# Kernel tuning notes

Hardware: AMD Instinct MI355X
Metric: run time of the kernel (lower is better)

The kernel has to match this reference:

```python
import jax, jax.numpy as jnp
import numpy as np

B, S, D, H, L, FF = 4, 2048, 256, 8, 4, 512
DK = D // H
EPS = 1e-5


def _ln(x, scale, bias):
    m = jnp.mean(x, axis=-1, keepdims=True)
    v = jnp.mean(jnp.square(x - m), axis=-1, keepdims=True)
    return (x - m) / jnp.sqrt(v + EPS) * scale + bias


def setup_inputs() -> dict:
    key = jax.random.key(0)
    ks = jax.random.split(key, 12)
    w = lambda k, shape: jax.random.normal(k, shape, dtype=jnp.float32) * 0.02
    return {
        "x": jax.random.normal(ks[0], (B, S, D), dtype=jnp.float32),
        "ln0_s": jnp.ones((D,), jnp.float32), "ln0_b": jnp.zeros((D,), jnp.float32),
        "ln1_s": jnp.ones((L, D), jnp.float32), "ln1_b": jnp.zeros((L, D), jnp.float32),
        "ln2_s": jnp.ones((L, D), jnp.float32), "ln2_b": jnp.zeros((L, D), jnp.float32),
        "wq": w(ks[1], (L, D, D)), "bq": jnp.zeros((L, D), jnp.float32),
        "wk": w(ks[2], (L, D, D)), "bk": jnp.zeros((L, D), jnp.float32),
        "wv": w(ks[3], (L, D, D)), "bv": jnp.zeros((L, D), jnp.float32),
        "wo": w(ks[4], (L, D, D)), "bo": jnp.zeros((L, D), jnp.float32),
        "w1": w(ks[5], (L, D, FF)), "b1": jnp.zeros((L, FF), jnp.float32),
        "w2": w(ks[6], (L, FF, D)), "b2": jnp.zeros((L, D), jnp.float32),
    }


def reference(x, ln0_s, ln0_b, ln1_s, ln1_b, ln2_s, ln2_b,
              wq, bq, wk, bk, wv, bv, wo, bo, w1, b1, w2, b2):
    scale = 1.0 / np.sqrt(DK).astype(np.float32)
    x = _ln(x, ln0_s, ln0_b)  # Encoder's leading LayerNorm

    def step(h, p):
        (l1s, l1b, l2s, l2b, Wq, Bq, Wk, Bk, Wv, Bv, Wo, Bo, W1, B1, W2, B2) = p
        # --- pre-norm multi-head attention ---
        x2 = _ln(h, l1s, l1b)
        q = (x2 @ Wq + Bq).reshape(B, S, H, DK)
        k = (x2 @ Wk + Bk).reshape(B, S, H, DK)
        v = (x2 @ Wv + Bv).reshape(B, S, H, DK)
        scores = jnp.einsum('bqhd,bkhd->bhqk', q, k) * scale  # [B,H,S,S]
        attn = jax.nn.softmax(scores, axis=-1)
        o = jnp.einsum('bhqk,bkhd->bqhd', attn, v).reshape(B, S, D)
        h = h + (o @ Wo + Bo)
        # --- pre-norm feed-forward (hidden fixed at 512, ReLU) ---
        x2 = _ln(h, l2s, l2b)
        h = h + (jax.nn.relu(x2 @ W1 + B1) @ W2 + B2)
        return h, None

    layer_params = (ln1_s, ln1_b, ln2_s, ln2_b, wq, bq, wk, bk,
                    wv, bv, wo, bo, w1, b1, w2, b2)
    x, _ = jax.lax.scan(step, x, layer_params)
    return x
```

## Files before the change

### kernel.cpp

```cpp
#include <hip/hip_runtime.h>
#include <hip/hip_bf16.h>
#include <math.h>

#define SEQ 2048
#define DIM 256
#define NH 8
#define DK 32
#define FF 512

typedef __bf16 bf16_t;
typedef bf16_t bf16x8 __attribute__((ext_vector_type(8)));
typedef bf16_t bf16x4 __attribute__((ext_vector_type(4)));
typedef float f32x4 __attribute__((ext_vector_type(4)));

#define QK_SCALE_LOG2 0.25503226632462494f
#if __has_builtin(__builtin_amdgcn_exp2f)
#define FAST_EXP2(x) __builtin_amdgcn_exp2f(x)
#else
#define FAST_EXP2(x) __expf((x) * 0.6931471805599453f)
#endif

template <int OUT_BF>
__global__ __launch_bounds__(256) void ln_kernel(
    const float* __restrict__ x, const float* __restrict__ s,
    const float* __restrict__ b, float* __restrict__ outf,
    bf16_t* __restrict__ outb) {
  int wave = threadIdx.x >> 6;
  int lane = threadIdx.x & 63;
  int row = blockIdx.x * 4 + wave;
  const float* xr = x + (size_t)row * DIM + lane * 4;
  float4 xv = *(const float4*)xr;
  float sum = xv.x + xv.y + xv.z + xv.w;
  float sq = xv.x * xv.x + xv.y * xv.y + xv.z * xv.z + xv.w * xv.w;
#pragma unroll
  for (int off = 1; off < 64; off <<= 1) {
    sum += __shfl_xor(sum, off);
    sq += __shfl_xor(sq, off);
  }
  float mean = sum * (1.0f / 256.0f);
  float var = sq * (1.0f / 256.0f) - mean * mean;
  float inv = rsqrtf(var + 1e-5f);
  float4 sv = *(const float4*)(s + lane * 4);
  float4 bv = *(const float4*)(b + lane * 4);
  float4 o;
  o.x = (xv.x - mean) * inv * sv.x + bv.x;
  o.y = (xv.y - mean) * inv * sv.y + bv.y;
  o.z = (xv.z - mean) * inv * sv.z + bv.z;
  o.w = (xv.w - mean) * inv * sv.w + bv.w;
  if (OUT_BF) {
    bf16x4 ob = {(bf16_t)o.x, (bf16_t)o.y, (bf16_t)o.z, (bf16_t)o.w};
    *(bf16x4*)(outb + (size_t)row * DIM + lane * 4) = ob;
  } else {
    *(float4*)(outf + (size_t)row * DIM + lane * 4) = o;
  }
}

__global__ __launch_bounds__(256) void wtrans_all_kernel(
    const float* __restrict__ wq, const float* __restrict__ wk,
    const float* __restrict__ wv, const float* __restrict__ wo,
    const float* __restrict__ w1, const float* __restrict__ w2,
    bf16_t* __restrict__ WqT, bf16_t* __restrict__ WkT,
    bf16_t* __restrict__ WvT, bf16_t* __restrict__ WoT,
    bf16_t* __restrict__ W1T, bf16_t* __restrict__ W2T) {
  __shared__ float tile[64][65];
  int idx = blockIdx.x;
  int layer = idx >> 7;
  int r = idx & 127;
  const float* src;
  bf16_t* dst;
  int N, k0, n0;
  if (r < 64) {
    int which = r >> 4, t = r & 15;
    N = 256;
    k0 = (t & 3) * 64;
    n0 = (t >> 2) * 64;
    src = (which == 0 ? wq : which == 1 ? wk : which == 2 ? wv : wo) + (size_t)layer * 65536;
    dst = (which == 0 ? WqT : which == 1 ? WkT : which == 2 ? WvT : WoT) + (size_t)layer * 65536;
  } else if (r < 96) {
    int t = r - 64;
    N = 512;
    k0 = (t & 3) * 64;
    n0 = (t >> 2) * 64;
    src = w1 + (size_t)layer * 131072;
    dst = W1T + (size_t)layer * 131072;
  } else {
    int t = r - 96;
    N = 256;
    k0 = (t & 7) * 64;
    n0 = (t >> 3) * 64;
    src = w2 + (size_t)layer * 131072;
    dst = W2T + (size_t)layer * 131072;
  }
  int K = (r >= 96) ? 512 : 256;

  int tr = threadIdx.x >> 4;
  int tc4 = (threadIdx.x & 15) * 4;
#pragma unroll
  for (int i = 0; i < 4; i++) {
    int kl = i * 16 + tr;
    float4 v = *(const float4*)(src + (size_t)(k0 + kl) * N + n0 + tc4);
    tile[kl][tc4 + 0] = v.x; tile[kl][tc4 + 1] = v.y;
    tile[kl][tc4 + 2] = v.z; tile[kl][tc4 + 3] = v.w;
  }
  __syncthreads();
#pragma unroll
  for (int i = 0; i < 4; i++) {
    int nl = i * 16 + tr;
    bf16x4 o = {(bf16_t)tile[tc4 + 0][nl], (bf16_t)tile[tc4 + 1][nl],
                (bf16_t)tile[tc4 + 2][nl], (bf16_t)tile[tc4 + 3][nl]};
    *(bf16x4*)(dst + (size_t)(n0 + nl) * K + k0 + tc4) = o;
  }
}

__device__ __forceinline__ void stage_tile(const bf16_t* __restrict__ src,
                                           bf16_t* dst, int tid, int ldk, int k0) {
#pragma unroll
  for (int u = 0; u < 2; u++) {
    int i = u * 256 + tid;
    int m = i >> 3, cd = i & 7, cs = cd ^ (m & 7);
    const bf16_t* g = src + (size_t)m * ldk + k0 + cs * 8;
    __builtin_amdgcn_global_load_lds(
        (const __attribute__((address_space(1))) unsigned int*)g,
        (__attribute__((address_space(3))) unsigned int*)(dst + i * 8),
        16, 0, 0);
  }
}

template <int K>
__device__ __forceinline__ void gemm7_body(
    const bf16_t* __restrict__ A, const bf16_t* __restrict__ BT,
    int m0, int n0, int tid, bf16_t* As, bf16_t* Bs, f32x4 (&acc)[2][2]) {
  const int lane = tid & 63;
  const int n16 = lane & 15, quad = lane >> 4;
  const int w = tid >> 6;
  const int mw = (w >> 1) * 32, nw = (w & 1) * 32;
  const int sw = n16 & 7;
  const bf16_t* Arow = A + (size_t)m0 * K;
  const bf16_t* Brow = BT + (size_t)n0 * K;

  stage_tile(Arow, As, tid, K, 0);
  stage_tile(Brow, Bs, tid, K, 0);
  __syncthreads();

  const int steps = K / 64;
#pragma unroll
  for (int s = 0; s < steps; s++) {
    int buf = s & 1;
    if (s + 1 < steps) {
      stage_tile(Arow, As + (buf ^ 1) * 4096, tid, K, (s + 1) * 64);
      stage_tile(Brow, Bs + (buf ^ 1) * 4096, tid, K, (s + 1) * 64);
    }
    const bf16_t* a = As + buf * 4096;
    const bf16_t* b = Bs + buf * 4096;
    bf16x8 af[2][2], bfv[2][2];
#pragma unroll
    for (int t = 0; t < 2; t++)
#pragma unroll
      for (int ks = 0; ks < 2; ks++) {
        int cd = (ks * 4 + quad) ^ sw;
        af[t][ks] = *(const bf16x8*)(a + (mw + t * 16 + n16) * 64 + cd * 8);
        bfv[t][ks] = *(const bf16x8*)(b + (nw + t * 16 + n16) * 64 + cd * 8);
      }
#pragma unroll
    for (int ks = 0; ks < 2; ks++)
#pragma unroll
      for (int mt = 0; mt < 2; mt++)
#pragma unroll
        for (int nt = 0; nt < 2; nt++)
          acc[mt][nt] = __builtin_amdgcn_mfma_f32_16x16x32_bf16(
              af[mt][ks], bfv[nt][ks], acc[mt][nt], 0, 0, 0);
    __syncthreads();
  }
}

template <int MODE, int N, int K>
__global__ __launch_bounds__(256) void gemm7_kernel(
    const bf16_t* __restrict__ A, const bf16_t* __restrict__ BT,
    const float* __restrict__ bias, const float* __restrict__ resid,
    float* __restrict__ outf, bf16_t* __restrict__ outb) {
  __shared__ __align__(16) bf16_t As[2 * 4096];
  __shared__ __align__(16) bf16_t Bs[2 * 4096];
  int tid = threadIdx.x;
  int lane = tid & 63;
  int n16 = lane & 15, quad = lane >> 4;
  int w = tid >> 6;
  int m0 = blockIdx.y * 64, n0 = blockIdx.x * 64;
  f32x4 acc[2][2] = {};
  gemm7_body<K>(A, BT, m0, n0, tid, As, Bs, acc);

  int m_base = m0 + (w >> 1) * 32;
  int n_base = n0 + (w & 1) * 32;
  float bias_v[2];
#pragma unroll
  for (int nt = 0; nt < 2; nt++) bias_v[nt] = bias[n_base + nt * 16 + n16];
#pragma unroll
  for (int mt = 0; mt < 2; mt++)
#pragma unroll
    for (int nt = 0; nt < 2; nt++) {
      int n = n_base + nt * 16 + n16;
#pragma unroll
      for (int r = 0; r < 4; r++) {
        int m = m_base + mt * 16 + quad * 4 + r;
        float val = acc[mt][nt][r] + bias_v[nt];
        if (MODE == 0) {
          size_t idx = (size_t)m * N + n;
          outf[idx] = resid[idx] + val;
        } else {
          outb[(size_t)m * N + n] = (bf16_t)fmaxf(val, 0.0f);
        }
      }
    }
}

__global__ __launch_bounds__(256) void qkv7_kernel(
    const bf16_t* __restrict__ A,
    const bf16_t* __restrict__ WqT, const bf16_t* __restrict__ WkT,
    const bf16_t* __restrict__ WvT,
    const float* __restrict__ bq, const float* __restrict__ bk,
    const float* __restrict__ bv,
    bf16_t* __restrict__ qo, bf16_t* __restrict__ ko,
    bf16_t* __restrict__ vo) {
  __shared__ __align__(16) bf16_t As[2 * 4096];
  __shared__ __align__(16) bf16_t Bs[2 * 4096];
  int which = blockIdx.x >> 2;
  int nblk = blockIdx.x & 3;
  const bf16_t* BT = (which == 0) ? WqT : (which == 1) ? WkT : WvT;
  const float* bias = (which == 0) ? bq : (which == 1) ? bk : bv;

  int tid = threadIdx.x;
  int lane = tid & 63;
  int n16 = lane & 15, quad = lane >> 4;
  int w = tid >> 6;
  int m0 = blockIdx.y * 64, n0 = nblk * 64;
  f32x4 acc[2][2] = {};
  gemm7_body<256>(A, BT, m0, n0, tid, As, Bs, acc);

  int m_base = m0 + (w >> 1) * 32;
  int n_base = n0 + (w & 1) * 32;
  float bias_v[2];
#pragma unroll
  for (int nt = 0; nt < 2; nt++) bias_v[nt] = bias[n_base + nt * 16 + n16];

#pragma unroll
  for (int mt = 0; mt < 2; mt++)
#pragma unroll
    for (int nt = 0; nt < 2; nt++) {
      int n = n_base + nt * 16 + n16;
      int hh = n >> 5, dk = n & 31;
      if (which == 2) {
        int s0 = m_base + mt * 16 + quad * 4;
        int bb = s0 >> 11, ss0 = s0 & 2047;
        bf16x4 o;
#pragma unroll
        for (int r = 0; r < 4; r++) o[r] = (bf16_t)(acc[mt][nt][r] + bias_v[nt]);
        *(bf16x4*)(vo + ((size_t)(bb * NH + hh) * DK + dk) * SEQ + ss0) = o;
      } else {
        bf16_t* dst = (which == 0) ? qo : ko;
        float sc = (which == 0) ? QK_SCALE_LOG2 : 1.0f;
#pragma unroll
        for (int r = 0; r < 4; r++) {
          int m = m_base + mt * 16 + quad * 4 + r;
          int bb = m >> 11, ss = m & 2047;
          dst[((size_t)(bb * NH + hh) * SEQ + ss) * DK + dk] =
              (bf16_t)((acc[mt][nt][r] + bias_v[nt]) * sc);
        }
      }
    }
}

__global__ __launch_bounds__(128) void flash6_kernel(
    const bf16_t* __restrict__ Q, const bf16_t* __restrict__ K,
    const bf16_t* __restrict__ VT, bf16_t* __restrict__ OB) {
  __shared__ __align__(16) bf16_t Plds[2][2][32][72];
  int bh = blockIdx.x;
  int q0 = blockIdx.y * 64;
  int w = threadIdx.x >> 6;
  int lane = threadIdx.x & 63;
  int n16 = lane & 15;
  int quad = lane >> 4;

  const bf16_t* Qb = Q + (size_t)bh * SEQ * DK;
  const bf16_t* Kb = K + (size_t)bh * SEQ * DK;
  const bf16_t* Vb = VT + (size_t)bh * DK * SEQ;
  int qr0 = q0 + w * 32;

  bf16x8 qfrag[2];
#pragma unroll
  for (int qg = 0; qg < 2; qg++)
    qfrag[qg] = *(const bf16x8*)(Qb + (size_t)(qr0 + qg * 16 + n16) * DK + quad * 8);

  bf16_t one = (bf16_t)1.0f;
  bf16x8 ones = {one, one, one, one, one, one, one, one};

  f32x4 oacc[2][2] = {};
  f32x4 lacc[2] = {};

#pragma unroll 2
  for (int kb0 = 0; kb0 < SEQ; kb0 += 64) {
    int buf = (kb0 >> 6) & 1;
    bf16x8 kf[4];
#pragma unroll
    for (int t = 0; t < 4; t++)
      kf[t] = *(const bf16x8*)(Kb + (size_t)(kb0 + t * 16 + n16) * DK + quad * 8);
    bf16x8 vf[2][2];
#pragma unroll
    for (int c = 0; c < 2; c++) {
      vf[c][0] = *(const bf16x8*)(Vb + (size_t)n16 * SEQ + kb0 + c * 32 + quad * 8);
      vf[c][1] = *(const bf16x8*)(Vb + (size_t)(16 + n16) * SEQ + kb0 + c * 32 + quad * 8);
    }
#pragma unroll
    for (int qg = 0; qg < 2; qg++) {
#pragma unroll
      for (int t = 0; t < 4; t++) {
        f32x4 sc = __builtin_amdgcn_mfma_f32_16x16x32_bf16(
            kf[t], qfrag[qg], (f32x4){0.f, 0.f, 0.f, 0.f}, 0, 0, 0);
        bf16x4 pf;
#pragma unroll
        for (int r = 0; r < 4; r++) pf[r] = (bf16_t)FAST_EXP2(sc[r]);
        *(bf16x4*)&Plds[buf][w][qg * 16 + n16][t * 16 + quad * 4] = pf;
      }
    }
#pragma unroll
    for (int qg = 0; qg < 2; qg++)
#pragma unroll
      for (int c = 0; c < 2; c++) {
        bf16x8 pf8 = *(const bf16x8*)&Plds[buf][w][qg * 16 + n16][c * 32 + quad * 8];
        lacc[qg] = __builtin_amdgcn_mfma_f32_16x16x32_bf16(pf8, ones, lacc[qg], 0, 0, 0);
        oacc[qg][0] = __builtin_amdgcn_mfma_f32_16x16x32_bf16(pf8, vf[c][0], oacc[qg][0], 0, 0, 0);
        oacc[qg][1] = __builtin_amdgcn_mfma_f32_16x16x32_bf16(pf8, vf[c][1], oacc[qg][1], 0, 0, 0);
      }
  }

  int bb = bh >> 3, hh = bh & 7;
#pragma unroll
  for (int qg = 0; qg < 2; qg++)
#pragma unroll
    for (int r = 0; r < 4; r++) {
      float linv = 1.0f / lacc[qg][r];
      int row = qr0 + qg * 16 + quad * 4 + r;
      bf16_t* op = OB + ((size_t)(bb * SEQ + row)) * DIM + hh * DK;
      op[n16] = (bf16_t)(oacc[qg][0][r] * linv);
      op[16 + n16] = (bf16_t)(oacc[qg][1][r] * linv);
    }
}

extern "C" void kernel_launch(void* const* d_in, const int* in_sizes, int n_in,
                              void* d_out, int out_size, void* d_ws, size_t ws_size,
                              hipStream_t stream) {
  const float* x     = (const float*)d_in[0];
  const float* ln0_s = (const float*)d_in[1];
  const float* ln0_b = (const float*)d_in[2];
  const float* ln1_s = (const float*)d_in[3];
  const float* ln1_b = (const float*)d_in[4];
  const float* ln2_s = (const float*)d_in[5];
  const float* ln2_b = (const float*)d_in[6];
  const float* wq = (const float*)d_in[7];
  const float* bq = (const float*)d_in[8];
  const float* wk = (const float*)d_in[9];
  const float* bk = (const float*)d_in[10];
  const float* wv = (const float*)d_in[11];
  const float* bv = (const float*)d_in[12];
  const float* wo = (const float*)d_in[13];
  const float* bo = (const float*)d_in[14];
  const float* w1 = (const float*)d_in[15];
  const float* b1 = (const float*)d_in[16];
  const float* w2 = (const float*)d_in[17];
  const float* b2 = (const float*)d_in[18];

  float* out = (float*)d_out;
  const size_t ACT = (size_t)8192 * DIM;

  bf16_t* wsb = (bf16_t*)d_ws;
  bf16_t* x2b = wsb;
  bf16_t* obf = x2b + ACT;
  bf16_t* qbf = obf + ACT;
  bf16_t* kbf = qbf + ACT;
  bf16_t* vbf = kbf + ACT;
  bf16_t* h1b = vbf + ACT;
  bf16_t* WqT = h1b + 2 * ACT;
  bf16_t* WkT = WqT + 4 * 65536;
  bf16_t* WvT = WkT + 4 * 65536;
  bf16_t* WoT = WvT + 4 * 65536;
  bf16_t* W1T = WoT + 4 * 65536;
  bf16_t* W2T = W1T + 4 * 131072;

  dim3 blk(256);
  dim3 blkF(128);
  dim3 gLN(2048);
  dim3 gG256(4, 128);
  dim3 gG512(8, 128);
  dim3 gQKV(12, 128);
  dim3 gAtt(32, 32);

  wtrans_all_kernel<<<dim3(512), blk, 0, stream>>>(wq, wk, wv, wo, w1, w2,
                                                   WqT, WkT, WvT, WoT, W1T, W2T);

  ln_kernel<0><<<gLN, blk, 0, stream>>>(x, ln0_s, ln0_b, out, nullptr);

  for (int l = 0; l < 4; l++) {
    bf16_t* WqTl = WqT + (size_t)l * 65536;
    bf16_t* WkTl = WkT + (size_t)l * 65536;
    bf16_t* WvTl = WvT + (size_t)l * 65536;
    bf16_t* WoTl = WoT + (size_t)l * 65536;
    bf16_t* W1Tl = W1T + (size_t)l * 131072;
    bf16_t* W2Tl = W2T + (size_t)l * 131072;

    ln_kernel<1><<<gLN, blk, 0, stream>>>(out, ln1_s + l * DIM, ln1_b + l * DIM, nullptr, x2b);
    qkv7_kernel<<<gQKV, blk, 0, stream>>>(x2b, WqTl, WkTl, WvTl,
                                          bq + l * DIM, bk + l * DIM, bv + l * DIM,
                                          qbf, kbf, vbf);
    flash6_kernel<<<gAtt, blkF, 0, stream>>>(qbf, kbf, vbf, obf);
    gemm7_kernel<0, 256, 256><<<gG256, blk, 0, stream>>>(obf, WoTl, bo + l * DIM, out, out, nullptr);
    ln_kernel<1><<<gLN, blk, 0, stream>>>(out, ln2_s + l * DIM, ln2_b + l * DIM, nullptr, x2b);
    gemm7_kernel<1, 512, 256><<<gG512, blk, 0, stream>>>(x2b, W1Tl, b1 + l * FF, nullptr, nullptr, h1b);
    gemm7_kernel<0, 256, 512><<<gG256, blk, 0, stream>>>(h1b, W2Tl, b2 + l * DIM, out, out, nullptr);
  }
}
```

Baseline: 468.8 us.

## Stage full K=256 slab in LDS for GEMMs and prefetch K/V in attention

The GEMM kernels drop the double-buffered 64-wide K loop. They now load all four K-chunks (256 wide) into LDS in a single stage, then compute without per-step barriers. The K=512 case does this twice. The attention kernel software-pipelines its K/V fragment loads by fetching the next block's fragments into registers while the current block is computed. This removes most barriers and hides global load latency, at the cost of 64KB of LDS per GEMM block and more registers in attention, which may reduce occupancy.

After: 468.2 us. About the same (-0.1%).

```diff
diff --git a/kernel.cpp b/kernel.cpp
--- a/kernel.cpp
+++ b/kernel.cpp
@@ -112,84 +112,76 @@
   }
 }
 
-__device__ __forceinline__ void stage_tile(const bf16_t* __restrict__ src,
-                                           bf16_t* dst, int tid, int ldk, int k0) {
-#pragma unroll
-  for (int u = 0; u < 2; u++) {
-    int i = u * 256 + tid;
-    int m = i >> 3, cd = i & 7, cs = cd ^ (m & 7);
-    const bf16_t* g = src + (size_t)m * ldk + k0 + cs * 8;
-    __builtin_amdgcn_global_load_lds(
-        (const __attribute__((address_space(1))) unsigned int*)g,
-        (__attribute__((address_space(3))) unsigned int*)(dst + i * 8),
-        16, 0, 0);
-  }
-}
-
-template <int K>
-__device__ __forceinline__ void gemm7_body(
-    const bf16_t* __restrict__ A, const bf16_t* __restrict__ BT,
-    int m0, int n0, int tid, bf16_t* As, bf16_t* Bs, f32x4 (&acc)[2][2]) {
-  const int lane = tid & 63;
-  const int n16 = lane & 15, quad = lane >> 4;
-  const int w = tid >> 6;
-  const int mw = (w >> 1) * 32, nw = (w & 1) * 32;
+__device__ __forceinline__ void stage4(const bf16_t* __restrict__ src,
+                                       bf16_t* dst, int tid, int ldk, int kofs) {
+#pragma unroll
+  for (int st = 0; st < 4; st++) {
+#pragma unroll
+    for (int u = 0; u < 2; u++) {
+      int i = u * 256 + tid;
+      int m = i >> 3, cd = i & 7, cs = cd ^ (m & 7);
+      const bf16_t* g = src + (size_t)m * ldk + kofs + st * 64 + cs * 8;
+      __builtin_amdgcn_global_load_lds(
+          (const __attribute__((address_space(1))) unsigned int*)g,
+          (__attribute__((address_space(3))) unsigned int*)(dst + st * 4096 + i * 8),
+          16, 0, 0);
+    }
+  }
+}
+
+__device__ __forceinline__ void compute4(const bf16_t* As, const bf16_t* Bs,
+                                         int mw, int nw, int n16, int quad,
+                                         f32x4 (&acc)[2][2]) {
   const int sw = n16 & 7;
-  const bf16_t* Arow = A + (size_t)m0 * K;
-  const bf16_t* Brow = BT + (size_t)n0 * K;
-
-  stage_tile(Arow, As, tid, K, 0);
-  stage_tile(Brow, Bs, tid, K, 0);
-  __syncthreads();
-
-  const int steps = K / 64;
-#pragma unroll
-  for (int s = 0; s < steps; s++) {
-    int buf = s & 1;
-    if (s + 1 < steps) {
-      stage_tile(Arow, As + (buf ^ 1) * 4096, tid, K, (s + 1) * 64);
-      stage_tile(Brow, Bs + (buf ^ 1) * 4096, tid, K, (s + 1) * 64);
-    }
-    const bf16_t* a = As + buf * 4096;
-    const bf16_t* b = Bs + buf * 4096;
-    bf16x8 af[2][2], bfv[2][2];
-#pragma unroll
-    for (int t = 0; t < 2; t++)
-#pragma unroll
-      for (int ks = 0; ks < 2; ks++) {
-        int cd = (ks * 4 + quad) ^ sw;
-        af[t][ks] = *(const bf16x8*)(a + (mw + t * 16 + n16) * 64 + cd * 8);
-        bfv[t][ks] = *(const bf16x8*)(b + (nw + t * 16 + n16) * 64 + cd * 8);
-      }
-#pragma unroll
-    for (int ks = 0; ks < 2; ks++)
-#pragma unroll
-      for (int mt = 0; mt < 2; mt++)
-#pragma unroll
-        for (int nt = 0; nt < 2; nt++)
-          acc[mt][nt] = __builtin_amdgcn_mfma_f32_16x16x32_bf16(
-              af[mt][ks], bfv[nt][ks], acc[mt][nt], 0, 0, 0);
-    __syncthreads();
+#pragma unroll
+  for (int st = 0; st < 4; st++) {
+#pragma unroll
+    for (int ks = 0; ks < 2; ks++) {
+      int cd = (ks * 4 + quad) ^ sw;
+      bf16x8 a0 = *(const bf16x8*)(As + st * 4096 + (mw + n16) * 64 + cd * 8);
+      bf16x8 a1 = *(const bf16x8*)(As + st * 4096 + (mw + 16 + n16) * 64 + cd * 8);
+      bf16x8 b0 = *(const bf16x8*)(Bs + st * 4096 + (nw + n16) * 64 + cd * 8);
+      bf16x8 b1 = *(const bf16x8*)(Bs + st * 4096 + (nw + 16 + n16) * 64 + cd * 8);
+      acc[0][0] = __builtin_amdgcn_mfma_f32_16x16x32_bf16(a0, b0, acc[0][0], 0, 0, 0);
+      acc[0][1] = __builtin_amdgcn_mfma_f32_16x16x32_bf16(a0, b1, acc[0][1], 0, 0, 0);
+      acc[1][0] = __builtin_amdgcn_mfma_f32_16x16x32_bf16(a1, b0, acc[1][0], 0, 0, 0);
+      acc[1][1] = __builtin_amdgcn_mfma_f32_16x16x32_bf16(a1, b1, acc[1][1], 0, 0, 0);
+    }
   }
 }
 
 template <int MODE, int N, int K>
-__global__ __launch_bounds__(256) void gemm7_kernel(
+__global__ __launch_bounds__(256) void gemm8_kernel(
     const bf16_t* __restrict__ A, const bf16_t* __restrict__ BT,
     const float* __restrict__ bias, const float* __restrict__ resid,
     float* __restrict__ outf, bf16_t* __restrict__ outb) {
-  __shared__ __align__(16) bf16_t As[2 * 4096];
-  __shared__ __align__(16) bf16_t Bs[2 * 4096];
+  __shared__ __align__(16) bf16_t As[16384];
+  __shared__ __align__(16) bf16_t Bs[16384];
   int tid = threadIdx.x;
   int lane = tid & 63;
   int n16 = lane & 15, quad = lane >> 4;
   int w = tid >> 6;
   int m0 = blockIdx.y * 64, n0 = blockIdx.x * 64;
+  int mw = (w >> 1) * 32, nw = (w & 1) * 32;
   f32x4 acc[2][2] = {};
-  gemm7_body<K>(A, BT, m0, n0, tid, As, Bs, acc);
-
-  int m_base = m0 + (w >> 1) * 32;
-  int n_base = n0 + (w & 1) * 32;
+
+  const bf16_t* Arow = A + (size_t)m0 * K;
+  const bf16_t* Brow = BT + (size_t)n0 * K;
+
+  stage4(Arow, As, tid, K, 0);
+  stage4(Brow, Bs, tid, K, 0);
+  __syncthreads();
+  compute4(As, Bs, mw, nw, n16, quad, acc);
+  if (K == 512) {
+    __syncthreads();
+    stage4(Arow, As, tid, K, 256);
+    stage4(Brow, Bs, tid, K, 256);
+    __syncthreads();
+    compute4(As, Bs, mw, nw, n16, quad, acc);
+  }
+
+  int m_base = m0 + mw;
+  int n_base = n0 + nw;
   float bias_v[2];
 #pragma unroll
   for (int nt = 0; nt < 2; nt++) bias_v[nt] = bias[n_base + nt * 16 + n16];
@@ -212,7 +204,7 @@
     }
 }
 
-__global__ __launch_bounds__(256) void qkv7_kernel(
+__global__ __launch_bounds__(256) void qkv8_kernel(
     const bf16_t* __restrict__ A,
     const bf16_t* __restrict__ WqT, const bf16_t* __restrict__ WkT,
     const bf16_t* __restrict__ WvT,
@@ -220,8 +212,8 @@
     const float* __restrict__ bv,
     bf16_t* __restrict__ qo, bf16_t* __restrict__ ko,
     bf16_t* __restrict__ vo) {
-  __shared__ __align__(16) bf16_t As[2 * 4096];
-  __shared__ __align__(16) bf16_t Bs[2 * 4096];
+  __shared__ __align__(16) bf16_t As[16384];
+  __shared__ __align__(16) bf16_t Bs[16384];
   int which = blockIdx.x >> 2;
   int nblk = blockIdx.x & 3;
   const bf16_t* BT = (which == 0) ? WqT : (which == 1) ? WkT : WvT;
@@ -232,11 +224,16 @@
   int n16 = lane & 15, quad = lane >> 4;
   int w = tid >> 6;
   int m0 = blockIdx.y * 64, n0 = nblk * 64;
+  int mw = (w >> 1) * 32, nw = (w & 1) * 32;
   f32x4 acc[2][2] = {};
-  gemm7_body<256>(A, BT, m0, n0, tid, As, Bs, acc);
-
-  int m_base = m0 + (w >> 1) * 32;
-  int n_base = n0 + (w & 1) * 32;
+
+  stage4(A + (size_t)m0 * 256, As, tid, 256, 0);
+  stage4(BT + (size_t)n0 * 256, Bs, tid, 256, 0);
+  __syncthreads();
+  compute4(As, Bs, mw, nw, n16, quad, acc);
+
+  int m_base = m0 + mw;
+  int n_base = n0 + nw;
   float bias_v[2];
 #pragma unroll
   for (int nt = 0; nt < 2; nt++) bias_v[nt] = bias[n_base + nt * 16 + n16];
@@ -268,7 +265,7 @@
     }
 }
 
-__global__ __launch_bounds__(128) void flash6_kernel(
+__global__ __launch_bounds__(128) void flash7_kernel(
     const bf16_t* __restrict__ Q, const bf16_t* __restrict__ K,
     const bf16_t* __restrict__ VT, bf16_t* __restrict__ OB) {
   __shared__ __align__(16) bf16_t Plds[2][2][32][72];
@@ -295,25 +292,38 @@
   f32x4 oacc[2][2] = {};
   f32x4 lacc[2] = {};
 
+  bf16x8 kfc[4], vfc[2][2];
+#pragma unroll
+  for (int t = 0; t < 4; t++)
+    kfc[t] = *(const bf16x8*)(Kb + (size_t)(t * 16 + n16) * DK + quad * 8);
+#pragma unroll
+  for (int c = 0; c < 2; c++) {
+    vfc[c][0] = *(const bf16x8*)(Vb + (size_t)n16 * SEQ + c * 32 + quad * 8);
+    vfc[c][1] = *(const bf16x8*)(Vb + (size_t)(16 + n16) * SEQ + c * 32 + quad * 8);
+  }
+
 #pragma unroll 2
   for (int kb0 = 0; kb0 < SEQ; kb0 += 64) {
     int buf = (kb0 >> 6) & 1;
-    bf16x8 kf[4];
-#pragma unroll
-    for (int t = 0; t < 4; t++)
-      kf[t] = *(const bf16x8*)(Kb + (size_t)(kb0 + t * 16 + n16) * DK + quad * 8);
-    bf16x8 vf[2][2];
-#pragma unroll
-    for (int c = 0; c < 2; c++) {
-      vf[c][0] = *(const bf16x8*)(Vb + (size_t)n16 * SEQ + kb0 + c * 32 + quad * 8);
-      vf[c][1] = *(const bf16x8*)(Vb + (size_t)(16 + n16) * SEQ + kb0 + c * 32 + quad * 8);
+    int nb = kb0 + 64;
+    bool has_next = nb < SEQ;
+    bf16x8 kfn[4], vfn[2][2];
+    if (has_next) {
+#pragma unroll
+      for (int t = 0; t < 4; t++)
+        kfn[t] = *(const bf16x8*)(Kb + (size_t)(nb + t * 16 + n16) * DK + quad * 8);
+#pragma unroll
+      for (int c = 0; c < 2; c++) {
+        vfn[c][0] = *(const bf16x8*)(Vb + (size_t)n16 * SEQ + nb + c * 32 + quad * 8);
+        vfn[c][1] = *(const bf16x8*)(Vb + (size_t)(16 + n16) * SEQ + nb + c * 32 + quad * 8);
+      }
     }
 #pragma unroll
     for (int qg = 0; qg < 2; qg++) {
 #pragma unroll
       for (int t = 0; t < 4; t++) {
         f32x4 sc = __builtin_amdgcn_mfma_f32_16x16x32_bf16(
-            kf[t], qfrag[qg], (f32x4){0.f, 0.f, 0.f, 0.f}, 0, 0, 0);
+            kfc[t], qfrag[qg], (f32x4){0.f, 0.f, 0.f, 0.f}, 0, 0, 0);
         bf16x4 pf;
 #pragma unroll
         for (int r = 0; r < 4; r++) pf[r] = (bf16_t)FAST_EXP2(sc[r]);
@@ -326,9 +336,18 @@
       for (int c = 0; c < 2; c++) {
         bf16x8 pf8 = *(const bf16x8*)&Plds[buf][w][qg * 16 + n16][c * 32 + quad * 8];
         lacc[qg] = __builtin_amdgcn_mfma_f32_16x16x32_bf16(pf8, ones, lacc[qg], 0, 0, 0);
-        oacc[qg][0] = __builtin_amdgcn_mfma_f32_16x16x32_bf16(pf8, vf[c][0], oacc[qg][0], 0, 0, 0);
-        oacc[qg][1] = __builtin_amdgcn_mfma_f32_16x16x32_bf16(pf8, vf[c][1], oacc[qg][1], 0, 0, 0);
-      }
+        oacc[qg][0] = __builtin_amdgcn_mfma_f32_16x16x32_bf16(pf8, vfc[c][0], oacc[qg][0], 0, 0, 0);
+        oacc[qg][1] = __builtin_amdgcn_mfma_f32_16x16x32_bf16(pf8, vfc[c][1], oacc[qg][1], 0, 0, 0);
+      }
+    if (has_next) {
+#pragma unroll
+      for (int t = 0; t < 4; t++) kfc[t] = kfn[t];
+#pragma unroll
+      for (int c = 0; c < 2; c++) {
+        vfc[c][0] = vfn[c][0];
+        vfc[c][1] = vfn[c][1];
+      }
+    }
   }
 
   int bb = bh >> 3, hh = bh & 7;
@@ -406,13 +425,13 @@
     bf16_t* W2Tl = W2T + (size_t)l * 131072;
 
     ln_kernel<1><<<gLN, blk, 0, stream>>>(out, ln1_s + l * DIM, ln1_b + l * DIM, nullptr, x2b);
-    qkv7_kernel<<<gQKV, blk, 0, stream>>>(x2b, WqTl, WkTl, WvTl,
+    qkv8_kernel<<<gQKV, blk, 0, stream>>>(x2b, WqTl, WkTl, WvTl,
                                           bq + l * DIM, bk + l * DIM, bv + l * DIM,
                                           qbf, kbf, vbf);
-    flash6_kernel<<<gAtt, blkF, 0, stream>>>(qbf, kbf, vbf, obf);
-    gemm7_kernel<0, 256, 256><<<gG256, blk, 0, stream>>>(obf, WoTl, bo + l * DIM, out, out, nullptr);
+    flash7_kernel<<<gAtt, blkF, 0, stream>>>(qbf, kbf, vbf, obf);
+    gemm8_kernel<0, 256, 256><<<gG256, blk, 0, stream>>>(obf, WoTl, bo + l * DIM, out, out, nullptr);
     ln_kernel<1><<<gLN, blk, 0, stream>>>(out, ln2_s + l * DIM, ln2_b + l * DIM, nullptr, x2b);
-    gemm7_kernel<1, 512, 256><<<gG512, blk, 0, stream>>>(x2b, W1Tl, b1 + l * FF, nullptr, nullptr, h1b);
-    gemm7_kernel<0, 256, 512><<<gG256, blk, 0, stream>>>(h1b, W2Tl, b2 + l * DIM, out, out, nullptr);
-  }
-}
+    gemm8_kernel<1, 512, 256><<<gG512, blk, 0, stream>>>(x2b, W1Tl, b1 + l * FF, nullptr, nullptr, h1b);
+    gemm8_kernel<0, 256, 512><<<gG256, blk, 0, stream>>>(h1b, W2Tl, b2 + l * DIM, out, out, nullptr);
+  }
+}
```
